# Optimization experiments

Measured on AMD Instinct MI355X. Metric: run time of the kernel, lower is better.

## Reference

```python
import jax, jax.numpy as jnp
import numpy as np

N_NODES = 50000
N_EDGES = 600000
IN_C, HID, OUT_C, HEADS = 128, 64, 16, 4


def setup_inputs() -> dict:
    key = jax.random.key(0)
    ks = jax.random.split(key, 12)
    s = 1.0 / np.sqrt(HID)
    return {
        "x": jax.random.normal(ks[0], (N_NODES, IN_C), dtype=jnp.float32),
        "edge_index": jax.random.randint(ks[1], (2, N_EDGES), 0, N_NODES, dtype=jnp.int64),
        "W_lin": jax.random.normal(ks[2], (IN_C, HID), dtype=jnp.float32) / np.sqrt(IN_C),
        "b_lin": jnp.zeros((HID,), dtype=jnp.float32),
        "Wq": jax.random.normal(ks[3], (HID, HID), dtype=jnp.float32) * s,
        "bq": jnp.zeros((HID,), dtype=jnp.float32),
        "Wk": jax.random.normal(ks[4], (HID, HID), dtype=jnp.float32) * s,
        "bk": jnp.zeros((HID,), dtype=jnp.float32),
        "Wv": jax.random.normal(ks[5], (HID, HID), dtype=jnp.float32) * s,
        "bv": jnp.zeros((HID,), dtype=jnp.float32),
        "W_out": jax.random.normal(ks[6], (HID, OUT_C), dtype=jnp.float32) * s,
        "b_out": jnp.zeros((OUT_C,), dtype=jnp.float32),
    }


def _dna_conv(xs, src, dst, norm, Wq, bq, Wk, bk, Wv, bv):
    # xs: [N, L, C] stacked layer histories. Multi-head attention per edge:
    # query = target node's latest layer, keys/values = source node's full history.
    N, L, C = xs.shape
    d = C // HEADS
    q = (xs[:, -1] @ Wq + bq).reshape(N, HEADS, d)          # [N,H,d]
    k = (xs @ Wk + bk).reshape(N, L, HEADS, d)               # [N,L,H,d]
    v = (xs @ Wv + bv).reshape(N, L, HEADS, d)
    scores = jnp.einsum('ehd,elhd->ehl', q[dst], k[src]) / jnp.sqrt(jnp.float32(d))
    attn = jax.nn.softmax(scores, axis=-1)                   # softmax over layer history
    msg = jnp.einsum('ehl,elhd->ehd', attn, v[src]).reshape(-1, C)  # [E,C]
    msg = msg * norm[:, None]                                # GCN symmetric norm
    return jax.ops.segment_sum(msg, dst, num_segments=N)


def reference(x, edge_index, W_lin, b_lin, Wq, bq, Wk, bk, Wv, bv, W_out, b_out):
    N = x.shape[0]
    loop = jnp.arange(N, dtype=edge_index.dtype)
    src = jnp.concatenate([edge_index[0], loop])
    dst = jnp.concatenate([edge_index[1], loop])
    deg = jax.ops.segment_sum(jnp.ones_like(dst, dtype=x.dtype), dst, num_segments=N)
    dinv = jnp.where(deg > 0, jax.lax.rsqrt(jnp.maximum(deg, 1.0)), 0.0)
    norm = dinv[src] * dinv[dst]

    h = x @ W_lin + b_lin                                    # [N,HID]
    xs = h[:, None, :]
    for _ in range(3):
        out = _dna_conv(xs, src, dst, norm, Wq, bq, Wk, bk, Wv, bv)
        xs = jnp.concatenate([xs, out[:, None, :]], axis=1)
    return xs[:, -1] @ W_out + b_out                          # [N,OUT_C]
```

## Files before the change

### kernel.cpp

```cpp
#include <hip/hip_runtime.h>


__device__ inline unsigned short bf16_rne(float f) {
    unsigned int u = __float_as_uint(f);
    unsigned int r = u + 0x7FFFu + ((u >> 16) & 1u);
    return (unsigned short)(r >> 16);
}

__global__ __launch_bounds__(256) void hist_dst_k(const int* __restrict__ dst,
                                                  int* __restrict__ cnt, int E) {
    int e = blockIdx.x * 256 + threadIdx.x;
    if (e < E) atomicAdd(&cnt[dst[e]], 1);
}

__global__ __launch_bounds__(256) void scan1_k(const int* __restrict__ cnt,
                                               int* __restrict__ excl,
                                               int* __restrict__ aux,
                                               float* __restrict__ dinv, int N) {
    __shared__ int wtot[4];
    int b = blockIdx.x, t = threadIdx.x;
    int lane = t & 63, w = t >> 6;
    int base = b * 1024 + t * 4;
    int v0 = (base + 0 < N) ? cnt[base + 0] + 1 : 0;
    int v1 = (base + 1 < N) ? cnt[base + 1] + 1 : 0;
    int v2 = (base + 2 < N) ? cnt[base + 2] + 1 : 0;
    int v3 = (base + 3 < N) ? cnt[base + 3] + 1 : 0;
    if (base + 0 < N) dinv[base + 0] = rsqrtf((float)v0);
    if (base + 1 < N) dinv[base + 1] = rsqrtf((float)v1);
    if (base + 2 < N) dinv[base + 2] = rsqrtf((float)v2);
    if (base + 3 < N) dinv[base + 3] = rsqrtf((float)v3);
    int s = v0 + v1 + v2 + v3;
    int incl = s;
#pragma unroll
    for (int off = 1; off < 64; off <<= 1) {
        int u = __shfl_up(incl, off);
        if (lane >= off) incl += u;
    }
    if (lane == 63) wtot[w] = incl;
    __syncthreads();
    int wb = 0;
#pragma unroll
    for (int j = 0; j < 4; ++j) if (j < w) wb += wtot[j];
    int ex = wb + incl - s;
    if (base + 0 < N) excl[base + 0] = ex;
    if (base + 1 < N) excl[base + 1] = ex + v0;
    if (base + 2 < N) excl[base + 2] = ex + v0 + v1;
    if (base + 3 < N) excl[base + 3] = ex + v0 + v1 + v2;
    if (t == 0) aux[b] = wtot[0] + wtot[1] + wtot[2] + wtot[3];
}

__global__ __launch_bounds__(64) void scan_aux_k(int* __restrict__ aux, int nb,
                                                 int* __restrict__ total) {
    int lane = threadIdx.x;
    int v = (lane < nb) ? aux[lane] : 0;
    int incl = v;
#pragma unroll
    for (int off = 1; off < 64; off <<= 1) {
        int u = __shfl_up(incl, off);
        if (lane >= off) incl += u;
    }
    if (lane < nb) aux[lane] = incl - v;
    if (lane == 63) total[0] = incl;
}

__global__ __launch_bounds__(256) void scan_add_k(int* __restrict__ offs,
                                                  const int* __restrict__ aux,
                                                  int* __restrict__ cursor, int N) {
    int i = blockIdx.x * 256 + threadIdx.x;
    if (i < N) {
        int o = offs[i] + aux[i >> 10];
        offs[i] = o;
        cursor[i] = o;
    }
}

__global__ __launch_bounds__(256) void scatter_dst_k(const int* __restrict__ src,
                                                     const int* __restrict__ dst,
                                                     int* __restrict__ cursor,
                                                     int* __restrict__ src_sorted,
                                                     int E, int N) {
    int e = blockIdx.x * 256 + threadIdx.x;
    int M = E + N;
    if (e >= M) return;
    int s, d;
    if (e < E) { s = src[e]; d = dst[e]; }
    else       { s = d = e - E; }
    int pos = atomicAdd(&cursor[d], 1);
    src_sorted[pos] = s;
}

__global__ __launch_bounds__(256) void lin128_64_k(const float* __restrict__ x,
                                                   const float* __restrict__ W,
                                                   const float* __restrict__ b,
                                                   float* __restrict__ y, int N) {
    __shared__ float sW[128 * 64];
    __shared__ float sb[64];
    for (int i = threadIdx.x; i < 128 * 64; i += 256) sW[i] = W[i];
    if (threadIdx.x < 64) sb[threadIdx.x] = b[threadIdx.x];
    __syncthreads();
    int w = threadIdx.x >> 6, c = threadIdx.x & 63;
    int r0 = blockIdx.x * 16 + w * 4;
    if (r0 >= N) return;
    const float* xr[4];
#pragma unroll
    for (int j = 0; j < 4; ++j) {
        int r = r0 + j; if (r > N - 1) r = N - 1;
        xr[j] = x + (size_t)r * 128;
    }
    float acc[4];
#pragma unroll
    for (int j = 0; j < 4; ++j) acc[j] = sb[c];
    for (int k = 0; k < 128; ++k) {
        float wv = sW[k * 64 + c];
#pragma unroll
        for (int j = 0; j < 4; ++j) acc[j] = fmaf(xr[j][k], wv, acc[j]);
    }
#pragma unroll
    for (int j = 0; j < 4; ++j) {
        int r = r0 + j;
        if (r < N) y[(size_t)r * 64 + c] = acc[j];
    }
}

template <bool WRITE_V0>
__global__ __launch_bounds__(192) void proj_qkv_k(const float* __restrict__ X,
                                                  const float* __restrict__ Wq, const float* __restrict__ bq,
                                                  const float* __restrict__ Wk, const float* __restrict__ bk,
                                                  const float* __restrict__ Wv, const float* __restrict__ bv,
                                                  const float* __restrict__ dinv,
                                                  float* __restrict__ q,
                                                  unsigned int* __restrict__ PL,
                                                  unsigned short* __restrict__ V0,
                                                  int N, int l, int RPB) {
    int w = threadIdx.x >> 6;
    int c = threadIdx.x & 63;
    const float* W = (w == 0) ? Wq : (w == 1) ? Wk : Wv;
    const float* B = (w == 0) ? bq : (w == 1) ? bk : bv;
    float wr[64];
#pragma unroll
    for (int k = 0; k < 64; ++k) wr[k] = W[k * 64 + c];
    float bias = B[c];
    int r0 = blockIdx.x * RPB;
    int r1 = r0 + RPB; if (r1 > N) r1 = N;
    unsigned short* PLh = (unsigned short*)PL;
    for (int r = r0; r < r1; ++r) {
        float xv = X[(size_t)r * 64 + c];
        float a = bias;
#pragma unroll
        for (int k = 0; k < 64; ++k) {
            float xk = __int_as_float(__builtin_amdgcn_readlane(__float_as_int(xv), k));
            a = fmaf(xk, wr[k], a);
        }
        if (w == 0) {
            q[(size_t)r * 64 + c] = a * 0.25f;
        } else if (w == 1) {
            PLh[((size_t)r * 192 + l * 64 + c) * 2] = bf16_rne(a);
        } else {
            unsigned short vb = bf16_rne(a * dinv[r]);
            PLh[((size_t)r * 192 + l * 64 + c) * 2 + 1] = vb;
            if (WRITE_V0) V0[(size_t)r * 64 + c] = vb;
        }
    }
}

template <int L>
__global__ __launch_bounds__(256) void attn_dst_k(const int* __restrict__ offs,
                                                  const int* __restrict__ src_sorted,
                                                  const float* __restrict__ dinv,
                                                  const float* __restrict__ q,
                                                  const unsigned int* __restrict__ PL,
                                                  const unsigned short* __restrict__ V0,
                                                  float* __restrict__ out,
                                                  int N) {
    int d    = (blockIdx.x * 256 + threadIdx.x) >> 6;
    int lane = threadIdx.x & 63;
    if (d >= N) return;
    int beg = offs[d], end = offs[d + 1];
    float qv  = (L > 1) ? q[(size_t)d * 64 + lane] : 0.0f;
    float acc = 0.0f;

    for (int base = beg; base < end; base += 64) {
        int m = end - base;
        if (m > 64) m = 64;
        int sid = (base + lane < end) ? src_sorted[base + lane] : 0;
#pragma unroll 4
        for (int i = 0; i < m; ++i) {
            int s = __shfl(sid, i);
            if (L == 1) {
                acc += __uint_as_float((unsigned int)V0[(size_t)s * 64 + lane] << 16);
            } else if (L == 2) {
                const unsigned int* p = PL + (size_t)s * 192;
                unsigned int u0 = p[lane];
                unsigned int u1 = p[64 + lane];
                float k0 = __uint_as_float((u0 & 0xFFFFu) << 16);
                float v0 = __uint_as_float(u0 & 0xFFFF0000u);
                float k1 = __uint_as_float((u1 & 0xFFFFu) << 16);
                float v1 = __uint_as_float(u1 & 0xFFFF0000u);
                float p0 = qv * k0;
                float p1 = qv * k1;
#pragma unroll
                for (int mk = 8; mk >= 1; mk >>= 1) {
                    p0 += __shfl_xor(p0, mk);
                    p1 += __shfl_xor(p1, mk);
                }
                float e  = __expf(p1 - p0);
                float w0 = __builtin_amdgcn_rcpf(1.0f + e);
                float w1 = 1.0f - w0;
                acc = fmaf(w0, v0, acc);
                acc = fmaf(w1, v1, acc);
            } else {
                const unsigned int* p = PL + (size_t)s * 192;
                unsigned int u0 = p[lane];
                unsigned int u1 = p[64 + lane];
                unsigned int u2 = p[128 + lane];
                float k0 = __uint_as_float((u0 & 0xFFFFu) << 16);
                float v0 = __uint_as_float(u0 & 0xFFFF0000u);
                float k1 = __uint_as_float((u1 & 0xFFFFu) << 16);
                float v1 = __uint_as_float(u1 & 0xFFFF0000u);
                float k2 = __uint_as_float((u2 & 0xFFFFu) << 16);
                float v2 = __uint_as_float(u2 & 0xFFFF0000u);
                float p0 = qv * k0;
                float p1 = qv * k1;
                float p2 = qv * k2;
#pragma unroll
                for (int mk = 8; mk >= 1; mk >>= 1) {
                    p0 += __shfl_xor(p0, mk);
                    p1 += __shfl_xor(p1, mk);
                    p2 += __shfl_xor(p2, mk);
                }
                float mx = fmaxf(fmaxf(p0, p1), p2);
                float w0 = __expf(p0 - mx);
                float w1 = __expf(p1 - mx);
                float w2 = __expf(p2 - mx);
                float inv = __builtin_amdgcn_rcpf(w0 + w1 + w2);
                float msg = w0 * v0;
                msg = fmaf(w1, v1, msg);
                msg = fmaf(w2, v2, msg);
                acc = fmaf(msg, inv, acc);
            }
        }
    }
    out[(size_t)d * 64 + lane] = acc * dinv[d];
}

__global__ __launch_bounds__(256) void out_proj_k(const float* __restrict__ xs,
                                                  const float* __restrict__ W,
                                                  const float* __restrict__ b,
                                                  float* __restrict__ y, int N) {
    __shared__ float sW[64 * 16];
    __shared__ float sb[16];
    for (int i = threadIdx.x; i < 64 * 16; i += 256) sW[i] = W[i];
    if (threadIdx.x < 16) sb[threadIdx.x] = b[threadIdx.x];
    __syncthreads();
    int row = blockIdx.x * 16 + (threadIdx.x >> 4);
    int c   = threadIdx.x & 15;
    if (row >= N) return;
    const float* xr = xs + (size_t)row * 64;
    float acc = sb[c];
#pragma unroll 16
    for (int k = 0; k < 64; ++k) acc = fmaf(xr[k], sW[k * 16 + c], acc);
    y[(size_t)row * 16 + c] = acc;
}

extern "C" void kernel_launch(void* const* d_in, const int* in_sizes, int n_in,
                              void* d_out, int out_size, void* d_ws, size_t ws_size,
                              hipStream_t stream) {
    const float* x     = (const float*)d_in[0];
    const int*   ei    = (const int*)d_in[1];
    const float* W_lin = (const float*)d_in[2];
    const float* b_lin = (const float*)d_in[3];
    const float* Wq    = (const float*)d_in[4];
    const float* bq    = (const float*)d_in[5];
    const float* Wk    = (const float*)d_in[6];
    const float* bk    = (const float*)d_in[7];
    const float* Wv    = (const float*)d_in[8];
    const float* bv    = (const float*)d_in[9];
    const float* W_out = (const float*)d_in[10];
    const float* b_out = (const float*)d_in[11];
    float* out = (float*)d_out;

    const int N = in_sizes[0] / 128;
    const int E = in_sizes[1] / 2;
    const int M = E + N;
    const int* srcp = ei;
    const int* dstp = ei + E;

    char* wsb = (char*)d_ws;
    float*          dinv       = (float*)wsb;           wsb += (size_t)N * sizeof(float);
    int*            cnt        = (int*)wsb;             wsb += (size_t)N * sizeof(int);
    int*            offs       = (int*)wsb;             wsb += (size_t)(N + 1) * sizeof(int);
    int*            cursor     = (int*)wsb;             wsb += (size_t)N * sizeof(int);
    int*            aux        = (int*)wsb;             wsb += 64 * sizeof(int);
    int*            src_sorted = (int*)wsb;             wsb += (size_t)M * sizeof(int);
    float*          qb         = (float*)wsb;           wsb += (size_t)N * 64 * sizeof(float);
    unsigned int*   PL         = (unsigned int*)wsb;    wsb += (size_t)N * 192 * sizeof(unsigned int);
    unsigned short* V0p        = (unsigned short*)wsb;  wsb += (size_t)N * 64 * sizeof(unsigned short);
    float*          hA         = (float*)wsb;           wsb += (size_t)N * 64 * sizeof(float);
    float*          outb       = (float*)wsb;

    const int gN   = (N + 255) / 256;
    const int gE   = (E + 255) / 256;
    const int gM   = (M + 255) / 256;
    const int gRow = (N + 3) / 4;
    const int g16  = (N + 15) / 16;
    const int nb   = (N + 1023) / 1024;
    const int RPB  = 16;
    const int gP   = (N + RPB - 1) / RPB;

    hipMemsetAsync(cnt, 0, (size_t)N * sizeof(int), stream);
    hist_dst_k<<<gE, 256, 0, stream>>>(dstp, cnt, E);
    scan1_k<<<nb, 256, 0, stream>>>(cnt, offs, aux, dinv, N);
    scan_aux_k<<<1, 64, 0, stream>>>(aux, nb, offs + N);
    scan_add_k<<<gN, 256, 0, stream>>>(offs, aux, cursor, N);
    scatter_dst_k<<<gM, 256, 0, stream>>>(srcp, dstp, cursor, src_sorted, E, N);

    lin128_64_k<<<g16, 256, 0, stream>>>(x, W_lin, b_lin, hA, N);
    proj_qkv_k<true><<<gP, 192, 0, stream>>>(hA, Wq, bq, Wk, bk, Wv, bv, dinv,
                                             qb, PL, V0p, N, 0, RPB);

    attn_dst_k<1><<<gRow, 256, 0, stream>>>(offs, src_sorted, dinv, qb, PL, V0p, outb, N);
    proj_qkv_k<false><<<gP, 192, 0, stream>>>(outb, Wq, bq, Wk, bk, Wv, bv, dinv,
                                              qb, PL, V0p, N, 1, RPB);
    attn_dst_k<2><<<gRow, 256, 0, stream>>>(offs, src_sorted, dinv, qb, PL, V0p, outb, N);
    proj_qkv_k<false><<<gP, 192, 0, stream>>>(outb, Wq, bq, Wk, bk, Wv, bv, dinv,
                                              qb, PL, V0p, N, 2, RPB);
    attn_dst_k<3><<<gRow, 256, 0, stream>>>(offs, src_sorted, dinv, qb, PL, V0p, outb, N);

    out_proj_k<<<g16, 256, 0, stream>>>(outb, W_out, b_out, out, N);
}
```

Before: 495.2 us.

## Process attention per destination with 16-lane groups, vector loads and prefetch

```diff
diff --git a/kernel.cpp b/kernel.cpp
--- a/kernel.cpp
+++ b/kernel.cpp
@@ -6,6 +6,8 @@
     unsigned int r = u + 0x7FFFu + ((u >> 16) & 1u);
     return (unsigned short)(r >> 16);
 }
+__device__ inline float kf(unsigned int u) { return __uint_as_float(u << 16); }
+__device__ inline float vf(unsigned int u) { return __uint_as_float(u & 0xFFFF0000u); }
 
 __global__ __launch_bounds__(256) void hist_dst_k(const int* __restrict__ dst,
                                                   int* __restrict__ cnt, int E) {
@@ -164,7 +166,7 @@
 }
 
 template <int L>
-__global__ __launch_bounds__(256) void attn_dst_k(const int* __restrict__ offs,
+__global__ __launch_bounds__(256) void attn_g16_k(const int* __restrict__ offs,
                                                   const int* __restrict__ src_sorted,
                                                   const float* __restrict__ dinv,
                                                   const float* __restrict__ q,
@@ -172,75 +174,109 @@
                                                   const unsigned short* __restrict__ V0,
                                                   float* __restrict__ out,
                                                   int N) {
-    int d    = (blockIdx.x * 256 + threadIdx.x) >> 6;
-    int lane = threadIdx.x & 63;
+    int d  = (blockIdx.x * 256 + threadIdx.x) >> 4;
+    int gl = threadIdx.x & 15;
+    int gb = threadIdx.x & 48;
     if (d >= N) return;
     int beg = offs[d], end = offs[d + 1];
-    float qv  = (L > 1) ? q[(size_t)d * 64 + lane] : 0.0f;
-    float acc = 0.0f;
-
-    for (int base = beg; base < end; base += 64) {
+
+    float4 qv = make_float4(0.f, 0.f, 0.f, 0.f);
+    if (L > 1) qv = *(const float4*)(q + (size_t)d * 64 + gl * 4);
+
+    float a0 = 0.f, a1 = 0.f, a2 = 0.f, a3 = 0.f;
+
+    for (int base = beg; base < end; base += 16) {
         int m = end - base;
-        if (m > 64) m = 64;
-        int sid = (base + lane < end) ? src_sorted[base + lane] : 0;
-#pragma unroll 4
+        if (m > 16) m = 16;
+        int sid = (base + gl < end) ? src_sorted[base + gl] : 0;
+
+        uint4 A0, A1, A2, B0, B1, B2;
+        uint2 Av, Bv;
+        int s0 = __shfl(sid, gb);
+        if (L == 1) {
+            Av = *(const uint2*)(V0 + (size_t)s0 * 64 + gl * 4);
+        } else {
+            const uint4* pp = (const uint4*)(PL + (size_t)s0 * 192) + gl;
+            A0 = pp[0];
+            A1 = pp[16];
+            if (L > 2) A2 = pp[32];
+        }
+
         for (int i = 0; i < m; ++i) {
-            int s = __shfl(sid, i);
+            int nx = i + 1 < m ? i + 1 : m - 1;
+            int sn = __shfl(sid, gb + nx);
             if (L == 1) {
-                acc += __uint_as_float((unsigned int)V0[(size_t)s * 64 + lane] << 16);
-            } else if (L == 2) {
-                const unsigned int* p = PL + (size_t)s * 192;
-                unsigned int u0 = p[lane];
-                unsigned int u1 = p[64 + lane];
-                float k0 = __uint_as_float((u0 & 0xFFFFu) << 16);
-                float v0 = __uint_as_float(u0 & 0xFFFF0000u);
-                float k1 = __uint_as_float((u1 & 0xFFFFu) << 16);
-                float v1 = __uint_as_float(u1 & 0xFFFF0000u);
-                float p0 = qv * k0;
-                float p1 = qv * k1;
-#pragma unroll
-                for (int mk = 8; mk >= 1; mk >>= 1) {
-                    p0 += __shfl_xor(p0, mk);
-                    p1 += __shfl_xor(p1, mk);
+                Bv = *(const uint2*)(V0 + (size_t)sn * 64 + gl * 4);
+            } else {
+                const uint4* pp = (const uint4*)(PL + (size_t)sn * 192) + gl;
+                B0 = pp[0];
+                B1 = pp[16];
+                if (L > 2) B2 = pp[32];
+            }
+
+            if (L == 1) {
+                a0 += __uint_as_float((Av.x & 0xFFFFu) << 16);
+                a1 += __uint_as_float(Av.x & 0xFFFF0000u);
+                a2 += __uint_as_float((Av.y & 0xFFFFu) << 16);
+                a3 += __uint_as_float(Av.y & 0xFFFF0000u);
+            } else {
+                float p0 = qv.x * kf(A0.x);
+                p0 = fmaf(qv.y, kf(A0.y), p0);
+                p0 = fmaf(qv.z, kf(A0.z), p0);
+                p0 = fmaf(qv.w, kf(A0.w), p0);
+                float p1 = qv.x * kf(A1.x);
+                p1 = fmaf(qv.y, kf(A1.y), p1);
+                p1 = fmaf(qv.z, kf(A1.z), p1);
+                p1 = fmaf(qv.w, kf(A1.w), p1);
+                float p2 = 0.f;
+                if (L > 2) {
+                    p2 = qv.x * kf(A2.x);
+                    p2 = fmaf(qv.y, kf(A2.y), p2);
+                    p2 = fmaf(qv.z, kf(A2.z), p2);
+                    p2 = fmaf(qv.w, kf(A2.w), p2);
                 }
-                float e  = __expf(p1 - p0);
-                float w0 = __builtin_amdgcn_rcpf(1.0f + e);
-                float w1 = 1.0f - w0;
-                acc = fmaf(w0, v0, acc);
-                acc = fmaf(w1, v1, acc);
+                p0 += __shfl_xor(p0, 1); p0 += __shfl_xor(p0, 2);
+                p1 += __shfl_xor(p1, 1); p1 += __shfl_xor(p1, 2);
+                if (L > 2) { p2 += __shfl_xor(p2, 1); p2 += __shfl_xor(p2, 2); }
+                float w0, w1, w2 = 0.f;
+                if (L == 2) {
+                    float e = __expf(p1 - p0);
+                    w0 = __builtin_amdgcn_rcpf(1.0f + e);
+                    w1 = 1.0f - w0;
+                } else {
+                    float mx = fmaxf(fmaxf(p0, p1), p2);
+                    float e0 = __expf(p0 - mx);
+                    float e1 = __expf(p1 - mx);
+                    float e2 = __expf(p2 - mx);
+                    float inv = __builtin_amdgcn_rcpf(e0 + e1 + e2);
+                    w0 = e0 * inv; w1 = e1 * inv; w2 = e2 * inv;
+                }
+                a0 = fmaf(w0, vf(A0.x), a0);
+                a1 = fmaf(w0, vf(A0.y), a1);
+                a2 = fmaf(w0, vf(A0.z), a2);
+                a3 = fmaf(w0, vf(A0.w), a3);
+                a0 = fmaf(w1, vf(A1.x), a0);
+                a1 = fmaf(w1, vf(A1.y), a1);
+                a2 = fmaf(w1, vf(A1.z), a2);
+                a3 = fmaf(w1, vf(A1.w), a3);
+                if (L > 2) {
+                    a0 = fmaf(w2, vf(A2.x), a0);
+                    a1 = fmaf(w2, vf(A2.y), a1);
+                    a2 = fmaf(w2, vf(A2.z), a2);
+                    a3 = fmaf(w2, vf(A2.w), a3);
+                }
+            }
+            if (L == 1) {
+                Av = Bv;
             } else {
-                const unsigned int* p = PL + (size_t)s * 192;
-                unsigned int u0 = p[lane];
-                unsigned int u1 = p[64 + lane];
-                unsigned int u2 = p[128 + lane];
-                float k0 = __uint_as_float((u0 & 0xFFFFu) << 16);
-                float v0 = __uint_as_float(u0 & 0xFFFF0000u);
-                float k1 = __uint_as_float((u1 & 0xFFFFu) << 16);
-                float v1 = __uint_as_float(u1 & 0xFFFF0000u);
-                float k2 = __uint_as_float((u2 & 0xFFFFu) << 16);
-                float v2 = __uint_as_float(u2 & 0xFFFF0000u);
-                float p0 = qv * k0;
-                float p1 = qv * k1;
-                float p2 = qv * k2;
-#pragma unroll
-                for (int mk = 8; mk >= 1; mk >>= 1) {
-                    p0 += __shfl_xor(p0, mk);
-                    p1 += __shfl_xor(p1, mk);
-                    p2 += __shfl_xor(p2, mk);
-                }
-                float mx = fmaxf(fmaxf(p0, p1), p2);
-                float w0 = __expf(p0 - mx);
-                float w1 = __expf(p1 - mx);
-                float w2 = __expf(p2 - mx);
-                float inv = __builtin_amdgcn_rcpf(w0 + w1 + w2);
-                float msg = w0 * v0;
-                msg = fmaf(w1, v1, msg);
-                msg = fmaf(w2, v2, msg);
-                acc = fmaf(msg, inv, acc);
+                A0 = B0; A1 = B1;
+                if (L > 2) A2 = B2;
             }
         }
     }
-    out[(size_t)d * 64 + lane] = acc * dinv[d];
+    float dv = dinv[d];
+    *(float4*)(out + (size_t)d * 64 + gl * 4) =
+        make_float4(a0 * dv, a1 * dv, a2 * dv, a3 * dv);
 }
 
 __global__ __launch_bounds__(256) void out_proj_k(const float* __restrict__ xs,
@@ -301,7 +337,6 @@
     const int gN   = (N + 255) / 256;
     const int gE   = (E + 255) / 256;
     const int gM   = (M + 255) / 256;
-    const int gRow = (N + 3) / 4;
     const int g16  = (N + 15) / 16;
     const int nb   = (N + 1023) / 1024;
     const int RPB  = 16;
@@ -318,13 +353,13 @@
     proj_qkv_k<true><<<gP, 192, 0, stream>>>(hA, Wq, bq, Wk, bk, Wv, bv, dinv,
                                              qb, PL, V0p, N, 0, RPB);
 
-    attn_dst_k<1><<<gRow, 256, 0, stream>>>(offs, src_sorted, dinv, qb, PL, V0p, outb, N);
+    attn_g16_k<1><<<g16, 256, 0, stream>>>(offs, src_sorted, dinv, qb, PL, V0p, outb, N);
     proj_qkv_k<false><<<gP, 192, 0, stream>>>(outb, Wq, bq, Wk, bk, Wv, bv, dinv,
                                               qb, PL, V0p, N, 1, RPB);
-    attn_dst_k<2><<<gRow, 256, 0, stream>>>(offs, src_sorted, dinv, qb, PL, V0p, outb, N);
+    attn_g16_k<2><<<g16, 256, 0, stream>>>(offs, src_sorted, dinv, qb, PL, V0p, outb, N);
     proj_qkv_k<false><<<gP, 192, 0, stream>>>(outb, Wq, bq, Wk, bk, Wv, bv, dinv,
                                               qb, PL, V0p, N, 2, RPB);
-    attn_dst_k<3><<<gRow, 256, 0, stream>>>(offs, src_sorted, dinv, qb, PL, V0p, outb, N);
+    attn_g16_k<3><<<g16, 256, 0, stream>>>(offs, src_sorted, dinv, qb, PL, V0p, outb, N);
 
     out_proj_k<<<g16, 256, 0, stream>>>(outb, W_out, b_out, out, N);
 }
```

After: 441.5 us. -10.8%, faster.
